# Optimization experiments

Hardware: AMD Instinct MI355X
Metric: run time of the kernel (lower is better)

## Reference

```python
import jax, jax.numpy as jnp
import numpy as np

B, C, D, H, W = 2, 64, 8, 32, 32
QK = max(1, C // 8)  # intermediate dim for query/key 1x1x1 convs


def setup_inputs() -> dict:
    key = jax.random.key(0)
    ks = jax.random.split(key, 8)
    s = 0.05
    return {
        "x": jax.random.normal(ks[0], (B, C, D, H, W), dtype=jnp.float32),
        "Wq": jax.random.normal(ks[1], (QK, C), dtype=jnp.float32) * s,
        "bq": jax.random.normal(ks[2], (QK,), dtype=jnp.float32) * s,
        "Wk": jax.random.normal(ks[3], (QK, C), dtype=jnp.float32) * s,
        "bk": jax.random.normal(ks[4], (QK,), dtype=jnp.float32) * s,
        "Wv": jax.random.normal(ks[5], (C, C), dtype=jnp.float32) * s,
        "bv": jax.random.normal(ks[6], (C,), dtype=jnp.float32) * s,
        "gamma": jax.random.normal(ks[7], (1,), dtype=jnp.float32) * s,
    }


def reference(x, Wq, bq, Wk, bk, Wv, bv, gamma):
    b, c, d, h, w = x.shape
    n = d * h * w
    xf = x.reshape(b, c, n)  # (B, C, N)
    # 1x1x1 convs == per-position linear maps over channels
    q = jnp.einsum('oc,bcn->bon', Wq, xf) + bq[None, :, None]  # (B, QK, N)
    k = jnp.einsum('oc,bcn->bon', Wk, xf) + bk[None, :, None]  # (B, QK, N)
    v = jnp.einsum('oc,bcn->bon', Wv, xf) + bv[None, :, None]  # (B, C,  N)
    # energy[b, i, j] = q[b, :, i] . k[b, :, j]
    energy = jnp.einsum('bqi,bqj->bij', q, k)  # (B, N, N)
    attn = jax.nn.softmax(energy, axis=-1)
    # out[b, c, i] = sum_j v[b, c, j] * attn[b, i, j]
    out = jnp.einsum('bcj,bij->bci', v, attn)  # (B, C, N)
    out = out.reshape(b, c, d, h, w)
    return gamma[0] * out + x
```

## Files before the change

### kernel.cpp

```cpp
#include <hip/hip_runtime.h>


using f32x16 = __attribute__((ext_vector_type(16))) float;
using u32x4  = __attribute__((ext_vector_type(4))) unsigned int;

#define LOG2E 1.4426950408889634f

static __device__ __forceinline__ f32x16 mfma_z(u32x4 a, u32x4 b) {
  f32x16 d;
  asm("v_mfma_f32_32x32x16_bf16 %0, %1, %2, 0" : "=v"(d) : "v"(a), "v"(b));
  return d;
}
static __device__ __forceinline__ void mfma_acc(f32x16& d, u32x4 a, u32x4 b) {
  asm("v_mfma_f32_32x32x16_bf16 %0, %1, %2, %0" : "+v"(d) : "v"(a), "v"(b));
}
static __device__ __forceinline__ unsigned pkbf(float lo, float hi) {
  unsigned r;
  asm("v_cvt_pk_bf16_f32 %0, %1, %2" : "=v"(r) : "v"(lo), "v"(hi));
  return r;
}
static __device__ __forceinline__ void plswap(unsigned& a, unsigned& b) {
  asm("v_permlane32_swap_b32 %0, %1" : "+v"(a), "+v"(b));
}
static __device__ __forceinline__ float exp2_hw(float x) {
  return __builtin_amdgcn_exp2f(x);
}
static __device__ __forceinline__ unsigned f2bf(float f) {
  union { float f; unsigned u; } v; v.f = f;
  return (v.u + 0x7fffu + ((v.u >> 16) & 1u)) >> 16;
}
static __device__ __forceinline__ u32x4 pack8(const float* p) {
  u32x4 r;
  r[0] = f2bf(p[0]) | (f2bf(p[1]) << 16);
  r[1] = f2bf(p[2]) | (f2bf(p[3]) << 16);
  r[2] = f2bf(p[4]) | (f2bf(p[5]) << 16);
  r[3] = f2bf(p[6]) | (f2bf(p[7]) << 16);
  return r;
}

__global__ __launch_bounds__(128) void k_proj(
    const float* __restrict__ x,
    const float* __restrict__ Wq, const float* __restrict__ bq,
    const float* __restrict__ Wk, const float* __restrict__ bk,
    const float* __restrict__ Wv, const float* __restrict__ bv,
    u32x4* __restrict__ Qf, u32x4* __restrict__ Kf, u32x4* __restrict__ Vf) {
  __shared__ float sW[2][8][64];
  __shared__ float sb[2][8];
  __shared__ float sWv[4][64];
  __shared__ float sbv[4];
  const int tid = threadIdx.x;
  if (blockIdx.x < 256) {
    {
      float* wp = &sW[0][0][0];
      for (int i = tid; i < 512; i += 128) { wp[i] = Wq[i]; wp[512 + i] = Wk[i]; }
      if (tid < 8) { sb[0][tid] = bq[tid]; sb[1][tid] = bk[tid]; }
    }
    __syncthreads();
    const int b    = blockIdx.x >> 7;
    const int nb   = blockIdx.x & 127;
    const int lane = tid & 63;
    const int wv   = tid >> 6;
    const int ql   = lane & 31, ch = lane >> 5;
    const int n    = nb * 64 + wv * 32 + ql;
    const float* xp = x + ((size_t)b << 19) + n;
    float aq[8], ak[8];
    #pragma unroll
    for (int o = 0; o < 8; ++o) { aq[o] = 0.f; ak[o] = 0.f; }
    #pragma unroll
    for (int ci = 0; ci < 32; ci += 4) {
      const int c = ch * 32 + ci;
      float xv[4];
      #pragma unroll
      for (int j = 0; j < 4; ++j) xv[j] = xp[(size_t)(c + j) << 13];
      #pragma unroll
      for (int o = 0; o < 8; ++o) {
        const float4 wq = *(const float4*)&sW[0][o][c];
        const float4 wk = *(const float4*)&sW[1][o][c];
        aq[o] += wq.x * xv[0] + wq.y * xv[1] + wq.z * xv[2] + wq.w * xv[3];
        ak[o] += wk.x * xv[0] + wk.y * xv[1] + wk.z * xv[2] + wk.w * xv[3];
      }
    }
    #pragma unroll
    for (int o = 0; o < 8; ++o) {
      aq[o] += __shfl_xor(aq[o], 32, 64);
      ak[o] += __shfl_xor(ak[o], 32, 64);
    }
    if (ch == 0) {
      float q8[8], k8[8];
      #pragma unroll
      for (int o = 0; o < 8; ++o) {
        q8[o] = (aq[o] + sb[0][o]) * LOG2E;
        k8[o] = ak[o] + sb[1][o];
      }
      Qf[((size_t)b << 13) + n] = pack8(q8);
      Kf[((size_t)b << 13) + n] = pack8(k8);
    }
  } else {
    const int bid = blockIdx.x - 256;
    const int b   = bid >> 7;
    const int coq = (bid >> 3) & 15;
    const int ngc = bid & 7;
    const int ng  = ngc * 128 + tid;
    const int co  = coq * 4;
    for (int i = tid; i < 256; i += 128)
      sWv[i >> 6][i & 63] = Wv[(co + (i >> 6)) * 64 + (i & 63)];
    if (tid < 4) sbv[tid] = bv[co + tid];
    __syncthreads();
    float acc[4][8];
    #pragma unroll
    for (int i = 0; i < 4; ++i)
      #pragma unroll
      for (int e = 0; e < 8; ++e) acc[i][e] = 0.f;
    const float* xb = x + ((size_t)b << 19) + ((size_t)ng << 3);
    #pragma unroll 4
    for (int c = 0; c < 64; ++c) {
      const float4* xp = (const float4*)(xb + ((size_t)c << 13));
      const float4 x0 = xp[0];
      const float4 x1 = xp[1];
      #pragma unroll
      for (int i = 0; i < 4; ++i) {
        const float wv = sWv[i][c];
        acc[i][0] += wv * x0.x; acc[i][1] += wv * x0.y;
        acc[i][2] += wv * x0.z; acc[i][3] += wv * x0.w;
        acc[i][4] += wv * x1.x; acc[i][5] += wv * x1.y;
        acc[i][6] += wv * x1.z; acc[i][7] += wv * x1.w;
      }
    }
    #pragma unroll
    for (int i = 0; i < 4; ++i) {
      const int c = co + i;
      const float bias = sbv[i];
      float v8[8];
      #pragma unroll
      for (int e = 0; e < 8; ++e) v8[e] = acc[i][e] + bias;
      const int idx = ((b * 512 + (ng >> 1)) * 2 + (c >> 5)) * 64 + (ng & 1) * 32 + (c & 31);
      Vf[idx] = pack8(v8);
    }
  }
}

__global__ __launch_bounds__(512, 4) void k_attn(
    const u32x4* __restrict__ Qf, const u32x4* __restrict__ Kf, const u32x4* __restrict__ Vf,
    const float* __restrict__ x, const float* __restrict__ gamma, float* __restrict__ out) {
  __shared__ float sO[64][33];
  __shared__ float sl[32];
  const int tid  = threadIdx.x;
  const int b    = blockIdx.x >> 8;
  const int qb   = blockIdx.x & 255;
  const int i0   = qb * 32;
  const int w    = tid >> 6;
  const int lane = tid & 63;
  const int ql   = lane & 31;
  const int h    = lane >> 5;

  for (int i = tid; i < 64 * 33; i += 512) (&sO[0][0])[i] = 0.f;
  if (tid < 32) sl[tid] = 0.f;
  __syncthreads();

  u32x4 zer; zer[0] = 0u; zer[1] = 0u; zer[2] = 0u; zer[3] = 0u;
  const int qkbase = b * 8192;
  const u32x4 qf = (lane < 32) ? Qf[qkbase + i0 + lane] : zer;

  f32x16 acc0, acc1;
  #pragma unroll
  for (int r = 0; r < 16; ++r) { acc0[r] = 0.f; acc1[r] = 0.f; }
  float lacc = 0.f;

  const int jbase = qkbase + w * 1024;
  const u32x4* __restrict__ vbase = Vf + ((size_t)(b * 512 + w * 64) << 7) + lane;

  auto body = [&](const u32x4& kf, const u32x4* vf) {
    f32x16 sacc = mfma_z(kf, qf);
    float p[16];
    #pragma unroll
    for (int r = 0; r < 16; ++r) p[r] = exp2_hw(sacc[r]);
    lacc += (((p[0] + p[1]) + (p[2] + p[3])) + ((p[4] + p[5]) + (p[6] + p[7])))
          + (((p[8] + p[9]) + (p[10] + p[11])) + ((p[12] + p[13]) + (p[14] + p[15])));
    unsigned wd[4][2];
    #pragma unroll
    for (int qq = 0; qq < 4; ++qq) {
      wd[qq][0] = pkbf(p[4 * qq + 0], p[4 * qq + 1]);
      wd[qq][1] = pkbf(p[4 * qq + 2], p[4 * qq + 3]);
    }
    plswap(wd[0][0], wd[1][0]);
    plswap(wd[0][1], wd[1][1]);
    plswap(wd[2][0], wd[3][0]);
    plswap(wd[2][1], wd[3][1]);
    u32x4 pf0, pf1;
    pf0[0] = wd[0][0]; pf0[1] = wd[0][1]; pf0[2] = wd[1][0]; pf0[3] = wd[1][1];
    pf1[0] = wd[2][0]; pf1[1] = wd[2][1]; pf1[2] = wd[3][0]; pf1[3] = wd[3][1];
    mfma_acc(acc0, vf[0], pf0);
    mfma_acc(acc1, vf[1], pf0);
    mfma_acc(acc0, vf[2], pf1);
    mfma_acc(acc1, vf[3], pf1);
  };

  u32x4 kA, kB, vA[4], vB[4];
  kA = (lane < 32) ? Kf[jbase + lane] : zer;
  { const u32x4* vp = vbase;
    vA[0] = vp[0]; vA[1] = vp[64]; vA[2] = vp[128]; vA[3] = vp[192]; }
  #pragma unroll 1
  for (int it = 0; it < 32; it += 2) {
    kB = (lane < 32) ? Kf[jbase + (it + 1) * 32 + lane] : zer;
    { const u32x4* vp = vbase + (size_t)(it + 1) * 256;
      vB[0] = vp[0]; vB[1] = vp[64]; vB[2] = vp[128]; vB[3] = vp[192]; }
    body(kA, vA);
    const int n2 = (it + 2) & 31;
    kA = (lane < 32) ? Kf[jbase + n2 * 32 + lane] : zer;
    { const u32x4* vp = vbase + (size_t)n2 * 256;
      vA[0] = vp[0]; vA[1] = vp[64]; vA[2] = vp[128]; vA[3] = vp[192]; }
    body(kB, vB);
  }

  #pragma unroll
  for (int r = 0; r < 16; ++r) {
    const int cr = (r & 3) + 8 * (r >> 2) + 4 * h;
    atomicAdd(&sO[cr][ql], acc0[r]);
    atomicAdd(&sO[cr + 32][ql], acc1[r]);
  }
  atomicAdd(&sl[ql], lacc);
  __syncthreads();

  const float g  = gamma[0];
  const int   c  = tid >> 3;
  const int   qg = (tid & 7) * 4;
  const size_t base = (((size_t)b * 64 + c) << 13) + i0 + qg;
  const float4 xv = *(const float4*)&x[base];
  float4 o;
  o.x = g * (sO[c][qg + 0] / sl[qg + 0]) + xv.x;
  o.y = g * (sO[c][qg + 1] / sl[qg + 1]) + xv.y;
  o.z = g * (sO[c][qg + 2] / sl[qg + 2]) + xv.z;
  o.w = g * (sO[c][qg + 3] / sl[qg + 3]) + xv.w;
  *(float4*)&out[base] = o;
}

extern "C" void kernel_launch(void* const* d_in, const int* in_sizes, int n_in,
                              void* d_out, int out_size, void* d_ws, size_t ws_size,
                              hipStream_t stream) {
  const float* x  = (const float*)d_in[0];
  const float* Wq = (const float*)d_in[1];
  const float* bq = (const float*)d_in[2];
  const float* Wk = (const float*)d_in[3];
  const float* bk = (const float*)d_in[4];
  const float* Wv = (const float*)d_in[5];
  const float* bv = (const float*)d_in[6];
  const float* gm = (const float*)d_in[7];
  if (ws_size < 2621440u) return;
  char* ws = (char*)d_ws;
  u32x4* Qf = (u32x4*)(ws);
  u32x4* Kf = (u32x4*)(ws + (256 << 10));
  u32x4* Vf = (u32x4*)(ws + (512 << 10));
  float* out = (float*)d_out;

  k_proj<<<dim3(512), dim3(128), 0, stream>>>(x, Wq, bq, Wk, bk, Wv, bv, Qf, Kf, Vf);
  k_attn<<<dim3(512), dim3(512), 0, stream>>>(Qf, Kf, Vf, x, gm, out);
}
```

Baseline: 82.60 us.

## Process two query tiles per block to reuse K/V loads, use MFMA builtins

Each attention block now handles 64 queries instead of 32, so every K and V fragment loaded is used for two query tiles. This halves the K/V memory traffic per query and halves the grid to 256 blocks, with occupancy lowered to 2 blocks per CU. Inline-asm MFMA calls are replaced by compiler builtins so the scheduler can interleave them with the surrounding code. The cost is more accumulator registers, a larger shared-memory reduction, and fewer blocks to spread across CUs.

Measured after the change: 79.52 us. 3.7% less time.

```diff
diff --git a/kernel.cpp b/kernel.cpp
--- a/kernel.cpp
+++ b/kernel.cpp
@@ -3,16 +3,20 @@
 
 using f32x16 = __attribute__((ext_vector_type(16))) float;
 using u32x4  = __attribute__((ext_vector_type(4))) unsigned int;
+using bf16x8 = __attribute__((ext_vector_type(8))) short;
 
 #define LOG2E 1.4426950408889634f
 
 static __device__ __forceinline__ f32x16 mfma_z(u32x4 a, u32x4 b) {
-  f32x16 d;
-  asm("v_mfma_f32_32x32x16_bf16 %0, %1, %2, 0" : "=v"(d) : "v"(a), "v"(b));
-  return d;
+  f32x16 z;
+  #pragma unroll
+  for (int r = 0; r < 16; ++r) z[r] = 0.f;
+  return __builtin_amdgcn_mfma_f32_32x32x16_bf16(
+      __builtin_bit_cast(bf16x8, a), __builtin_bit_cast(bf16x8, b), z, 0, 0, 0);
 }
 static __device__ __forceinline__ void mfma_acc(f32x16& d, u32x4 a, u32x4 b) {
-  asm("v_mfma_f32_32x32x16_bf16 %0, %1, %2, %0" : "+v"(d) : "v"(a), "v"(b));
+  d = __builtin_amdgcn_mfma_f32_32x32x16_bf16(
+      __builtin_bit_cast(bf16x8, a), __builtin_bit_cast(bf16x8, b), d, 0, 0, 0);
 }
 static __device__ __forceinline__ unsigned pkbf(float lo, float hi) {
   unsigned r;
@@ -139,43 +143,45 @@
   }
 }
 
-__global__ __launch_bounds__(512, 4) void k_attn(
+__global__ __launch_bounds__(512, 2) void k_attn(
     const u32x4* __restrict__ Qf, const u32x4* __restrict__ Kf, const u32x4* __restrict__ Vf,
     const float* __restrict__ x, const float* __restrict__ gamma, float* __restrict__ out) {
-  __shared__ float sO[64][33];
-  __shared__ float sl[32];
+  __shared__ float sO[64][65];
+  __shared__ float sl[64];
   const int tid  = threadIdx.x;
-  const int b    = blockIdx.x >> 8;
-  const int qb   = blockIdx.x & 255;
-  const int i0   = qb * 32;
+  const int b    = blockIdx.x >> 7;
+  const int qb   = blockIdx.x & 127;
+  const int i0   = qb * 64;
   const int w    = tid >> 6;
   const int lane = tid & 63;
   const int ql   = lane & 31;
   const int h    = lane >> 5;
 
-  for (int i = tid; i < 64 * 33; i += 512) (&sO[0][0])[i] = 0.f;
-  if (tid < 32) sl[tid] = 0.f;
+  for (int i = tid; i < 64 * 65; i += 512) (&sO[0][0])[i] = 0.f;
+  if (tid < 64) sl[tid] = 0.f;
   __syncthreads();
 
   u32x4 zer; zer[0] = 0u; zer[1] = 0u; zer[2] = 0u; zer[3] = 0u;
   const int qkbase = b * 8192;
-  const u32x4 qf = (lane < 32) ? Qf[qkbase + i0 + lane] : zer;
-
-  f32x16 acc0, acc1;
-  #pragma unroll
-  for (int r = 0; r < 16; ++r) { acc0[r] = 0.f; acc1[r] = 0.f; }
-  float lacc = 0.f;
+  const u32x4 qf0 = (lane < 32) ? Qf[qkbase + i0 + lane] : zer;
+  const u32x4 qf1 = (lane < 32) ? Qf[qkbase + i0 + 32 + lane] : zer;
+
+  f32x16 acc00, acc01, acc10, acc11;
+  #pragma unroll
+  for (int r = 0; r < 16; ++r) { acc00[r] = 0.f; acc01[r] = 0.f; acc10[r] = 0.f; acc11[r] = 0.f; }
+  float lacc0 = 0.f, lacc1 = 0.f;
 
   const int jbase = qkbase + w * 1024;
   const u32x4* __restrict__ vbase = Vf + ((size_t)(b * 512 + w * 64) << 7) + lane;
 
-  auto body = [&](const u32x4& kf, const u32x4* vf) {
+  auto tile = [&](const u32x4& kf, const u32x4* vf, const u32x4& qf,
+                  f32x16& a0, f32x16& a1, float& lac) {
     f32x16 sacc = mfma_z(kf, qf);
     float p[16];
     #pragma unroll
     for (int r = 0; r < 16; ++r) p[r] = exp2_hw(sacc[r]);
-    lacc += (((p[0] + p[1]) + (p[2] + p[3])) + ((p[4] + p[5]) + (p[6] + p[7])))
-          + (((p[8] + p[9]) + (p[10] + p[11])) + ((p[12] + p[13]) + (p[14] + p[15])));
+    lac += (((p[0] + p[1]) + (p[2] + p[3])) + ((p[4] + p[5]) + (p[6] + p[7])))
+         + (((p[8] + p[9]) + (p[10] + p[11])) + ((p[12] + p[13]) + (p[14] + p[15])));
     unsigned wd[4][2];
     #pragma unroll
     for (int qq = 0; qq < 4; ++qq) {
@@ -189,10 +195,14 @@
     u32x4 pf0, pf1;
     pf0[0] = wd[0][0]; pf0[1] = wd[0][1]; pf0[2] = wd[1][0]; pf0[3] = wd[1][1];
     pf1[0] = wd[2][0]; pf1[1] = wd[2][1]; pf1[2] = wd[3][0]; pf1[3] = wd[3][1];
-    mfma_acc(acc0, vf[0], pf0);
-    mfma_acc(acc1, vf[1], pf0);
-    mfma_acc(acc0, vf[2], pf1);
-    mfma_acc(acc1, vf[3], pf1);
+    mfma_acc(a0, vf[0], pf0);
+    mfma_acc(a1, vf[1], pf0);
+    mfma_acc(a0, vf[2], pf1);
+    mfma_acc(a1, vf[3], pf1);
+  };
+  auto body = [&](const u32x4& kf, const u32x4* vf) {
+    tile(kf, vf, qf0, acc00, acc01, lacc0);
+    tile(kf, vf, qf1, acc10, acc11, lacc1);
   };
 
   u32x4 kA, kB, vA[4], vB[4];
@@ -215,23 +225,30 @@
   #pragma unroll
   for (int r = 0; r < 16; ++r) {
     const int cr = (r & 3) + 8 * (r >> 2) + 4 * h;
-    atomicAdd(&sO[cr][ql], acc0[r]);
-    atomicAdd(&sO[cr + 32][ql], acc1[r]);
-  }
-  atomicAdd(&sl[ql], lacc);
+    atomicAdd(&sO[cr][ql], acc00[r]);
+    atomicAdd(&sO[cr + 32][ql], acc01[r]);
+    atomicAdd(&sO[cr][32 + ql], acc10[r]);
+    atomicAdd(&sO[cr + 32][32 + ql], acc11[r]);
+  }
+  atomicAdd(&sl[ql], lacc0);
+  atomicAdd(&sl[32 + ql], lacc1);
   __syncthreads();
 
   const float g  = gamma[0];
   const int   c  = tid >> 3;
-  const int   qg = (tid & 7) * 4;
+  const int   qg = (tid & 7) * 8;
   const size_t base = (((size_t)b * 64 + c) << 13) + i0 + qg;
-  const float4 xv = *(const float4*)&x[base];
-  float4 o;
-  o.x = g * (sO[c][qg + 0] / sl[qg + 0]) + xv.x;
-  o.y = g * (sO[c][qg + 1] / sl[qg + 1]) + xv.y;
-  o.z = g * (sO[c][qg + 2] / sl[qg + 2]) + xv.z;
-  o.w = g * (sO[c][qg + 3] / sl[qg + 3]) + xv.w;
-  *(float4*)&out[base] = o;
+  #pragma unroll
+  for (int half = 0; half < 2; ++half) {
+    const int q4 = qg + half * 4;
+    const float4 xv = *(const float4*)&x[base + half * 4];
+    float4 o;
+    o.x = g * (sO[c][q4 + 0] / sl[q4 + 0]) + xv.x;
+    o.y = g * (sO[c][q4 + 1] / sl[q4 + 1]) + xv.y;
+    o.z = g * (sO[c][q4 + 2] / sl[q4 + 2]) + xv.z;
+    o.w = g * (sO[c][q4 + 3] / sl[q4 + 3]) + xv.w;
+    *(float4*)&out[base + half * 4] = o;
+  }
 }
 
 extern "C" void kernel_launch(void* const* d_in, const int* in_sizes, int n_in,
@@ -253,5 +270,5 @@
   float* out = (float*)d_out;
 
   k_proj<<<dim3(512), dim3(128), 0, stream>>>(x, Wq, bq, Wk, bk, Wv, bv, Qf, Kf, Vf);
-  k_attn<<<dim3(512), dim3(512), 0, stream>>>(Qf, Kf, Vf, x, gm, out);
-}
+  k_attn<<<dim3(256), dim3(512), 0, stream>>>(Qf, Kf, Vf, x, gm, out);
+}
```

## Split attention key range across two blocks with a separate combine kernel

Applied to the files above, without the earlier changes.

The attention kernel now splits each query block's key range into two halves, each processed by its own workgroup, which doubles the grid to 1024 blocks. Each block writes partial output and row sums to workspace, and a new combine kernel adds the halves, normalizes, and applies the gamma residual. Inline asm MFMA is replaced with compiler builtins and the launch bound occupancy hint rises to 8. The goal is more parallelism and occupancy on the GPU, paid for by an extra launch and a partial-result round trip through global memory. If the workspace is too small, the old single-kernel path is used instead.

Result: slower. 324.0 us (+292.2%).

```diff
diff --git a/kernel.cpp b/kernel.cpp
--- a/kernel.cpp
+++ b/kernel.cpp
@@ -3,16 +3,23 @@
 
 using f32x16 = __attribute__((ext_vector_type(16))) float;
 using u32x4  = __attribute__((ext_vector_type(4))) unsigned int;
+using bf16x8 = __attribute__((ext_vector_type(8))) short;
 
 #define LOG2E 1.4426950408889634f
+#define WS_BASE   2621440u
+#define SLOT_F    2080
+#define WS_SPLIT  (WS_BASE + 1024u * SLOT_F * 4u)
 
 static __device__ __forceinline__ f32x16 mfma_z(u32x4 a, u32x4 b) {
-  f32x16 d;
-  asm("v_mfma_f32_32x32x16_bf16 %0, %1, %2, 0" : "=v"(d) : "v"(a), "v"(b));
-  return d;
+  f32x16 z;
+  #pragma unroll
+  for (int r = 0; r < 16; ++r) z[r] = 0.f;
+  return __builtin_amdgcn_mfma_f32_32x32x16_bf16(
+      __builtin_bit_cast(bf16x8, a), __builtin_bit_cast(bf16x8, b), z, 0, 0, 0);
 }
 static __device__ __forceinline__ void mfma_acc(f32x16& d, u32x4 a, u32x4 b) {
-  asm("v_mfma_f32_32x32x16_bf16 %0, %1, %2, %0" : "+v"(d) : "v"(a), "v"(b));
+  d = __builtin_amdgcn_mfma_f32_32x32x16_bf16(
+      __builtin_bit_cast(bf16x8, a), __builtin_bit_cast(bf16x8, b), d, 0, 0, 0);
 }
 static __device__ __forceinline__ unsigned pkbf(float lo, float hi) {
   unsigned r;
@@ -139,7 +146,134 @@
   }
 }
 
-__global__ __launch_bounds__(512, 4) void k_attn(
+__global__ __launch_bounds__(512, 8) void k_attn(
+    const u32x4* __restrict__ Qf, const u32x4* __restrict__ Kf, const u32x4* __restrict__ Vf,
+    float* __restrict__ pO) {
+  __shared__ float sO[64][33];
+  __shared__ float sl[32];
+  const int tid  = threadIdx.x;
+  const int b    = blockIdx.x >> 9;
+  const int qb   = (blockIdx.x >> 1) & 255;
+  const int s    = blockIdx.x & 1;
+  const int i0   = qb * 32;
+  const int w    = tid >> 6;
+  const int lane = tid & 63;
+  const int ql   = lane & 31;
+  const int h    = lane >> 5;
+
+  for (int i = tid; i < 64 * 33; i += 512) (&sO[0][0])[i] = 0.f;
+  if (tid < 32) sl[tid] = 0.f;
+  __syncthreads();
+
+  u32x4 zer; zer[0] = 0u; zer[1] = 0u; zer[2] = 0u; zer[3] = 0u;
+  const int qkbase = b * 8192;
+  const u32x4 qf = (lane < 32) ? Qf[qkbase + i0 + lane] : zer;
+
+  f32x16 acc0, acc1;
+  #pragma unroll
+  for (int r = 0; r < 16; ++r) { acc0[r] = 0.f; acc1[r] = 0.f; }
+  float lacc = 0.f;
+
+  const int kofs  = s * 4096 + w * 512;
+  const int jbase = qkbase + kofs;
+  const u32x4* __restrict__ vbase = Vf + ((size_t)(b * 512 + (kofs >> 4)) << 7) + lane;
+
+  auto body = [&](const u32x4& kf, const u32x4* vf) {
+    f32x16 sacc = mfma_z(kf, qf);
+    float p[16];
+    #pragma unroll
+    for (int r = 0; r < 16; ++r) p[r] = exp2_hw(sacc[r]);
+    lacc += (((p[0] + p[1]) + (p[2] + p[3])) + ((p[4] + p[5]) + (p[6] + p[7])))
+          + (((p[8] + p[9]) + (p[10] + p[11])) + ((p[12] + p[13]) + (p[14] + p[15])));
+    unsigned wd[4][2];
+    #pragma unroll
+    for (int qq = 0; qq < 4; ++qq) {
+      wd[qq][0] = pkbf(p[4 * qq + 0], p[4 * qq + 1]);
+      wd[qq][1] = pkbf(p[4 * qq + 2], p[4 * qq + 3]);
+    }
+    plswap(wd[0][0], wd[1][0]);
+    plswap(wd[0][1], wd[1][1]);
+    plswap(wd[2][0], wd[3][0]);
+    plswap(wd[2][1], wd[3][1]);
+    u32x4 pf0, pf1;
+    pf0[0] = wd[0][0]; pf0[1] = wd[0][1]; pf0[2] = wd[1][0]; pf0[3] = wd[1][1];
+    pf1[0] = wd[2][0]; pf1[1] = wd[2][1]; pf1[2] = wd[3][0]; pf1[3] = wd[3][1];
+    mfma_acc(acc0, vf[0], pf0);
+    mfma_acc(acc1, vf[1], pf0);
+    mfma_acc(acc0, vf[2], pf1);
+    mfma_acc(acc1, vf[3], pf1);
+  };
+
+  u32x4 kA, kB, vA[4], vB[4];
+  kA = (lane < 32) ? Kf[jbase + lane] : zer;
+  { const u32x4* vp = vbase;
+    vA[0] = vp[0]; vA[1] = vp[64]; vA[2] = vp[128]; vA[3] = vp[192]; }
+  #pragma unroll 1
+  for (int it = 0; it < 16; it += 2) {
+    kB = (lane < 32) ? Kf[jbase + (it + 1) * 32 + lane] : zer;
+    { const u32x4* vp = vbase + (size_t)(it + 1) * 256;
+      vB[0] = vp[0]; vB[1] = vp[64]; vB[2] = vp[128]; vB[3] = vp[192]; }
+    body(kA, vA);
+    const int n2 = (it + 2) & 15;
+    kA = (lane < 32) ? Kf[jbase + n2 * 32 + lane] : zer;
+    { const u32x4* vp = vbase + (size_t)n2 * 256;
+      vA[0] = vp[0]; vA[1] = vp[64]; vA[2] = vp[128]; vA[3] = vp[192]; }
+    body(kB, vB);
+  }
+
+  #pragma unroll
+  for (int r = 0; r < 16; ++r) {
+    const int cr = (r & 3) + 8 * (r >> 2) + 4 * h;
+    atomicAdd(&sO[cr][ql], acc0[r]);
+    atomicAdd(&sO[cr + 32][ql], acc1[r]);
+  }
+  atomicAdd(&sl[ql], lacc);
+  __syncthreads();
+
+  float* slot = pO + (size_t)blockIdx.x * SLOT_F;
+  const int c  = tid >> 3;
+  const int qg = (tid & 7) * 4;
+  float4 o;
+  o.x = sO[c][qg + 0];
+  o.y = sO[c][qg + 1];
+  o.z = sO[c][qg + 2];
+  o.w = sO[c][qg + 3];
+  *(float4*)&slot[c * 32 + qg] = o;
+  if (tid < 32) slot[2048 + tid] = sl[tid];
+}
+
+__global__ __launch_bounds__(256) void k_combine(
+    const float* __restrict__ pO, const float* __restrict__ x,
+    const float* __restrict__ gamma, float* __restrict__ out) {
+  __shared__ float sl[32];
+  const int tid = threadIdx.x;
+  const int b   = blockIdx.x >> 8;
+  const int qb  = blockIdx.x & 255;
+  const int i0  = qb * 32;
+  const float* s0 = pO + (size_t)blockIdx.x * 2 * SLOT_F;
+  const float* s1 = s0 + SLOT_F;
+  if (tid < 32) sl[tid] = s0[2048 + tid] + s1[2048 + tid];
+  __syncthreads();
+  const float g  = gamma[0];
+  const int   c  = tid >> 2;
+  const int   qg = (tid & 3) * 8;
+  const size_t base = (((size_t)b * 64 + c) << 13) + i0 + qg;
+  #pragma unroll
+  for (int v = 0; v < 2; ++v) {
+    const int q4 = qg + v * 4;
+    const float4 o0 = *(const float4*)&s0[c * 32 + q4];
+    const float4 o1 = *(const float4*)&s1[c * 32 + q4];
+    const float4 xv = *(const float4*)&x[base + v * 4];
+    float4 o;
+    o.x = g * ((o0.x + o1.x) / sl[q4 + 0]) + xv.x;
+    o.y = g * ((o0.y + o1.y) / sl[q4 + 1]) + xv.y;
+    o.z = g * ((o0.z + o1.z) / sl[q4 + 2]) + xv.z;
+    o.w = g * ((o0.w + o1.w) / sl[q4 + 3]) + xv.w;
+    *(float4*)&out[base + v * 4] = o;
+  }
+}
+
+__global__ __launch_bounds__(512, 4) void k_attn_single(
     const u32x4* __restrict__ Qf, const u32x4* __restrict__ Kf, const u32x4* __restrict__ Vf,
     const float* __restrict__ x, const float* __restrict__ gamma, float* __restrict__ out) {
   __shared__ float sO[64][33];
@@ -152,23 +286,18 @@
   const int lane = tid & 63;
   const int ql   = lane & 31;
   const int h    = lane >> 5;
-
   for (int i = tid; i < 64 * 33; i += 512) (&sO[0][0])[i] = 0.f;
   if (tid < 32) sl[tid] = 0.f;
   __syncthreads();
-
   u32x4 zer; zer[0] = 0u; zer[1] = 0u; zer[2] = 0u; zer[3] = 0u;
   const int qkbase = b * 8192;
   const u32x4 qf = (lane < 32) ? Qf[qkbase + i0 + lane] : zer;
-
   f32x16 acc0, acc1;
   #pragma unroll
   for (int r = 0; r < 16; ++r) { acc0[r] = 0.f; acc1[r] = 0.f; }
   float lacc = 0.f;
-
   const int jbase = qkbase + w * 1024;
   const u32x4* __restrict__ vbase = Vf + ((size_t)(b * 512 + w * 64) << 7) + lane;
-
   auto body = [&](const u32x4& kf, const u32x4* vf) {
     f32x16 sacc = mfma_z(kf, qf);
     float p[16];
@@ -194,7 +323,6 @@
     mfma_acc(acc0, vf[2], pf1);
     mfma_acc(acc1, vf[3], pf1);
   };
-
   u32x4 kA, kB, vA[4], vB[4];
   kA = (lane < 32) ? Kf[jbase + lane] : zer;
   { const u32x4* vp = vbase;
@@ -211,7 +339,6 @@
       vA[0] = vp[0]; vA[1] = vp[64]; vA[2] = vp[128]; vA[3] = vp[192]; }
     body(kB, vB);
   }
-
   #pragma unroll
   for (int r = 0; r < 16; ++r) {
     const int cr = (r & 3) + 8 * (r >> 2) + 4 * h;
@@ -220,7 +347,6 @@
   }
   atomicAdd(&sl[ql], lacc);
   __syncthreads();
-
   const float g  = gamma[0];
   const int   c  = tid >> 3;
   const int   qg = (tid & 7) * 4;
@@ -245,13 +371,19 @@
   const float* Wv = (const float*)d_in[5];
   const float* bv = (const float*)d_in[6];
   const float* gm = (const float*)d_in[7];
-  if (ws_size < 2621440u) return;
+  if (ws_size < WS_BASE) return;
   char* ws = (char*)d_ws;
   u32x4* Qf = (u32x4*)(ws);
   u32x4* Kf = (u32x4*)(ws + (256 << 10));
   u32x4* Vf = (u32x4*)(ws + (512 << 10));
+  float* pO = (float*)(ws + WS_BASE);
   float* out = (float*)d_out;
 
   k_proj<<<dim3(512), dim3(128), 0, stream>>>(x, Wq, bq, Wk, bk, Wv, bv, Qf, Kf, Vf);
-  k_attn<<<dim3(512), dim3(512), 0, stream>>>(Qf, Kf, Vf, x, gm, out);
-}
+  if (ws_size >= WS_SPLIT) {
+    k_attn<<<dim3(1024), dim3(512), 0, stream>>>(Qf, Kf, Vf, pO);
+    k_combine<<<dim3(512), dim3(256), 0, stream>>>(pO, x, gm, out);
+  } else {
+    k_attn_single<<<dim3(512), dim3(512), 0, stream>>>(Qf, Kf, Vf, x, gm, out);
+  }
+}
```
